# Kernel tuning notes

Hardware: AMD Instinct MI355X
Metric: run time of the kernel (lower is better)

Reference implementation:

```python
import jax, jax.numpy as jnp
import numpy as np

B, S, D_MODEL, H = 2, 2048, 2048, 16
DQK = D_MODEL // H            # 128
DV = D_MODEL * 2 // H // 3    # 85 (GLU branch)
SCALE = DQK ** -0.5
ROPE_BASE = 10000.0


def apply_rope(x):
    # x: [B, S, H, D], NeoX-style half rotation
    D = x.shape[-1]
    half = D // 2
    inv_freq = 1.0 / (ROPE_BASE ** (jnp.arange(half, dtype=jnp.float32) / half))
    ang = jnp.arange(x.shape[1], dtype=jnp.float32)[:, None] * inv_freq[None, :]  # [S, half]
    cos = jnp.cos(ang)[None, :, None, :]
    sin = jnp.sin(ang)[None, :, None, :]
    x1, x2 = x[..., :half], x[..., half:]
    return jnp.concatenate([x1 * cos - x2 * sin, x2 * cos + x1 * sin], axis=-1)


def setup_inputs() -> dict:
    key = jax.random.key(0)
    ks = jax.random.split(key, 12)
    init = lambda k, shape, fan_in: jax.random.uniform(k, shape, jnp.float32, -1.0, 1.0) * (fan_in ** -0.5)
    q = jax.random.normal(ks[0], (B, S, D_MODEL), jnp.float32)
    k = jax.random.normal(ks[1], (B, S, D_MODEL), jnp.float32)
    v = jax.random.normal(ks[2], (B, S, D_MODEL), jnp.float32)
    # causal boolean mask: True = masked (upper triangle)
    mask = jnp.triu(jnp.ones((S, S), dtype=bool), k=1)
    Wq = init(ks[3], (D_MODEL, DQK * H), D_MODEL)
    bq = init(ks[4], (DQK * H,), D_MODEL)
    Wk = init(ks[5], (D_MODEL, DQK * H), D_MODEL)
    bk = init(ks[6], (DQK * H,), D_MODEL)
    Wv = init(ks[7], (D_MODEL, DV * H * 2), D_MODEL)
    bv = init(ks[8], (DV * H * 2,), D_MODEL)
    Wo = init(ks[9], (DV * H, D_MODEL), DV * H)
    bo = init(ks[10], (D_MODEL,), DV * H)
    return {"q": q, "k": k, "v": v, "mask": mask,
            "Wq": Wq, "bq": bq, "Wk": Wk, "bk": bk,
            "Wv": Wv, "bv": bv, "Wo": Wo, "bo": bo}


def reference(q, k, v, mask, Wq, bq, Wk, bk, Wv, bv, Wo, bo):
    qp = q @ Wq + bq                      # [B,S,H*DQK]
    kp = k @ Wk + bk                      # [B,S,H*DQK]
    vp = v @ Wv + bv                      # [B,S,2*H*DV]
    # GLU over the FULL last dim (matches torch chunk(2, dim=-1) before unflatten)
    half = DV * H
    vg = vp[..., :half] * jax.nn.silu(vp[..., half:])   # [B,S,H*DV]
    qh = qp.reshape(B, S, H, DQK)
    kh = kp.reshape(B, S, H, DQK)
    vh = vg.reshape(B, S, H, DV)
    qh = apply_rope(qh)
    kh = apply_rope(kh)
    # [B,H,S,D]
    qh = qh.transpose(0, 2, 1, 3)
    kh = kh.transpose(0, 2, 1, 3)
    vh = vh.transpose(0, 2, 1, 3)
    score = jnp.einsum('bhqd,bhkd->bhqk', qh, kh) * SCALE  # [B,H,S,S]
    score = jnp.where(mask[None, None, :, :], -jnp.inf, score)
    attn = jax.nn.softmax(score, axis=-1)
    o = jnp.einsum('bhqk,bhkd->bhqd', attn, vh)            # [B,H,S,DV]
    o = o.transpose(0, 2, 1, 3).reshape(B, S, H * DV)
    return o @ Wo + bo                                     # [B,S,D_MODEL]
```

## Files before the change

kernel.cpp:

```cpp
#include <hip/hip_runtime.h>
#include <cstdint>
#include <cmath>

typedef __bf16 bf16;
typedef __bf16 bf16x8 __attribute__((ext_vector_type(8)));
typedef float f32x4 __attribute__((ext_vector_type(4)));

#define B_      2
#define S_      2048
#define H_      16
#define DQK_    128
#define DV_     85
#define DVP_    96
#define DMODEL_ 2048
#define NKV_    1360
#define KH_     1536
#define NV_     2720
#define NVP_    2816
#define SCALE_  0.08838834764831845f
#define QSCALE_ 0.12752044442215615f
#define M2_     16.0f

__device__ __forceinline__ void lds_cp16(const void* g, void* l) {
    __builtin_amdgcn_global_load_lds(
        (const __attribute__((address_space(1))) unsigned int*)(uintptr_t)g,
        (__attribute__((address_space(3))) unsigned int*)(uintptr_t)l,
        16, 0, 0);
}

__global__ __launch_bounds__(256) void detect_dtype(const unsigned int* __restrict__ w,
                                                    int* __restrict__ flag) {
    __shared__ int cnt;
    if (threadIdx.x == 0) cnt = 0;
    __syncthreads();
    unsigned v = w[threadIdx.x];
    unsigned e = (v >> 7) & 0xFFu;
    if (e > 100u && e < 140u) atomicAdd(&cnt, 1);
    __syncthreads();
    if (threadIdx.x == 0) *flag = (cnt >= 200) ? 1 : 0;
}

__global__ __launch_bounds__(256) void norm_mat(const void* __restrict__ src, bf16* __restrict__ dst,
                                                const int* __restrict__ flag, long n8) {
    long i = (long)blockIdx.x * 256 + threadIdx.x;
    if (i >= n8) return;
    if (*flag) {
        ((bf16x8*)dst)[i] = ((const bf16x8*)src)[i];
    } else {
        const float* s = (const float*)src;
        bf16x8 v;
#pragma unroll
        for (int j = 0; j < 8; ++j) v[j] = (bf16)s[i * 8 + j];
        ((bf16x8*)dst)[i] = v;
    }
}

__global__ __launch_bounds__(256) void norm_bias4(
    const void* __restrict__ s0, const void* __restrict__ s1,
    const void* __restrict__ s2, const void* __restrict__ s3,
    float* __restrict__ d0, float* __restrict__ d1,
    float* __restrict__ d2, float* __restrict__ d3,
    const int* __restrict__ flag) {
    int j = blockIdx.x * 256 + threadIdx.x;
    const void* s; float* d;
    if (j < DMODEL_) { s = s0; d = d0; }
    else if ((j -= DMODEL_) < DMODEL_) { s = s1; d = d1; }
    else if ((j -= DMODEL_) < NV_) { s = s2; d = d2; }
    else if ((j -= NV_) < DMODEL_) { s = s3; d = d3; }
    else return;
    d[j] = (*flag) ? (float)((const bf16*)s)[j] : ((const float*)s)[j];
}

__global__ __launch_bounds__(256) void transpose_pad_dyn(
    const void* __restrict__ in, bf16* __restrict__ out, const int* __restrict__ flag,
    int R, int C, int Rp, int Cp) {
    __shared__ bf16 tile[32][33];
    const bool isbf = (*flag != 0);
    int r0 = blockIdx.x * 32, c0 = blockIdx.y * 32;
    int tx = threadIdx.x, ty = threadIdx.y;
#pragma unroll
    for (int i = 0; i < 32; i += 8) {
        int r = r0 + ty + i, c = c0 + tx;
        bf16 v = (bf16)0.0f;
        if (r < R && c < C) {
            size_t idx = (size_t)r * C + c;
            v = isbf ? ((const bf16*)in)[idx] : (bf16)((const float*)in)[idx];
        }
        tile[ty + i][tx] = v;
    }
    __syncthreads();
#pragma unroll
    for (int i = 0; i < 32; i += 8) {
        int oc = c0 + ty + i, orr = r0 + tx;
        if (oc < Cp && orr < Rp) out[(size_t)oc * Rp + orr] = tile[tx][ty + i];
    }
}

__global__ __launch_bounds__(256) void transpose_wo_dyn(
    const void* __restrict__ in, bf16* __restrict__ out, const int* __restrict__ flag) {
    __shared__ bf16 tile[32][33];
    const bool isbf = (*flag != 0);
    int k0 = blockIdx.x * 32, n0 = blockIdx.y * 32;
    int tx = threadIdx.x, ty = threadIdx.y;
#pragma unroll
    for (int i = 0; i < 32; i += 8) {
        int k = k0 + ty + i, c = n0 + tx;
        int hh = k / DVP_, dd = k - hh * DVP_;
        bf16 v = (bf16)0.0f;
        if (dd < DV_) {
            size_t idx = (size_t)(hh * DV_ + dd) * DMODEL_ + c;
            v = isbf ? ((const bf16*)in)[idx] : (bf16)((const float*)in)[idx];
        }
        tile[ty + i][tx] = v;
    }
    __syncthreads();
#pragma unroll
    for (int i = 0; i < 32; i += 8) {
        int n = n0 + ty + i, k = k0 + tx;
        out[(size_t)n * KH_ + k] = tile[tx][ty + i];
    }
}

__global__ __launch_bounds__(256) void gemm_bt(
    const bf16* __restrict__ A, const bf16* __restrict__ Bt,
    const float* __restrict__ bias, bf16* __restrict__ C,
    int M, int N, int K, int Nreal, int ldc) {
    __shared__ bf16 As[128 * 32];
    __shared__ bf16 Bs[128 * 32];
    const int t = threadIdx.x, lane = t & 63, w = t >> 6;
    const int m0 = blockIdx.x * 128, n0 = blockIdx.y * 128;
    const int wm = (w >> 1) * 64, wn = (w & 1) * 64;
    const int fm = lane & 15, quad = lane >> 4, fk = quad * 8;
    const int srow = lane >> 2, scol = (lane & 3) * 8;
    f32x4 acc[4][4] = {};
    for (int k0 = 0; k0 < K; k0 += 32) {
        __syncthreads();
#pragma unroll
        for (int j = 0; j < 2; ++j) {
            int c = j * 4 + w;
            lds_cp16(A + (size_t)(m0 + c * 16 + srow) * K + k0 + scol, &As[c * 512]);
            lds_cp16(Bt + (size_t)(n0 + c * 16 + srow) * K + k0 + scol, &Bs[c * 512]);
        }
        __syncthreads();
        bf16x8 af[4], bfr[4];
#pragma unroll
        for (int i = 0; i < 4; ++i) {
            af[i]  = *(const bf16x8*)&As[(wm + i * 16 + fm) * 32 + fk];
            bfr[i] = *(const bf16x8*)&Bs[(wn + i * 16 + fm) * 32 + fk];
        }
#pragma unroll
        for (int i = 0; i < 4; ++i)
#pragma unroll
            for (int jn = 0; jn < 4; ++jn)
                acc[i][jn] = __builtin_amdgcn_mfma_f32_16x16x32_bf16(af[i], bfr[jn], acc[i][jn], 0, 0, 0);
    }
#pragma unroll
    for (int jn = 0; jn < 4; ++jn) {
        int col = n0 + wn + jn * 16 + fm;
        if (col >= Nreal) continue;
        float bv = bias[col];
#pragma unroll
        for (int i = 0; i < 4; ++i) {
            int rowb = m0 + wm + i * 16 + quad * 4;
#pragma unroll
            for (int r = 0; r < 4; ++r)
                C[(size_t)(rowb + r) * ldc + col] = (bf16)(acc[i][jn][r] + bv);
        }
    }
}

__global__ __launch_bounds__(256) void gemm_bt_oh(
    const bf16* __restrict__ Oh, const bf16* __restrict__ Bt,
    const float* __restrict__ bias, bf16* __restrict__ C, float* __restrict__ Cf,
    const int* __restrict__ outflag) {
    __shared__ bf16 As[128 * 32];
    __shared__ bf16 Bs[128 * 32];
    const int t = threadIdx.x, lane = t & 63, w = t >> 6;
    const int m0 = blockIdx.x * 128, n0 = blockIdx.y * 128;
    const int wm = (w >> 1) * 64, wn = (w & 1) * 64;
    const int fm = lane & 15, quad = lane >> 4, fk = quad * 8;
    const int srow = lane >> 2, scol = (lane & 3) * 8;
    f32x4 acc[4][4] = {};
    for (int k0 = 0; k0 < KH_; k0 += 32) {
        __syncthreads();
#pragma unroll
        for (int j = 0; j < 2; ++j) {
            int c = j * 4 + w;
            int m = m0 + c * 16 + srow;
            int k = k0 + scol;
            int hh = k / DVP_, dd = k - hh * DVP_;
            const bf16* ga = Oh + ((size_t)((m >> 11) * H_ + hh) * S_ + (m & (S_ - 1))) * DVP_ + dd;
            lds_cp16(ga, &As[c * 512]);
            lds_cp16(Bt + (size_t)(n0 + c * 16 + srow) * KH_ + k0 + scol, &Bs[c * 512]);
        }
        __syncthreads();
        bf16x8 af[4], bfr[4];
#pragma unroll
        for (int i = 0; i < 4; ++i) {
            af[i]  = *(const bf16x8*)&As[(wm + i * 16 + fm) * 32 + fk];
            bfr[i] = *(const bf16x8*)&Bs[(wn + i * 16 + fm) * 32 + fk];
        }
#pragma unroll
        for (int i = 0; i < 4; ++i)
#pragma unroll
            for (int jn = 0; jn < 4; ++jn)
                acc[i][jn] = __builtin_amdgcn_mfma_f32_16x16x32_bf16(af[i], bfr[jn], acc[i][jn], 0, 0, 0);
    }
    bool bf16out = (*outflag != 0);
#pragma unroll
    for (int jn = 0; jn < 4; ++jn) {
        int col = n0 + wn + jn * 16 + fm;
        float bv = bias[col];
#pragma unroll
        for (int i = 0; i < 4; ++i) {
            int rowb = m0 + wm + i * 16 + quad * 4;
            if (bf16out) {
#pragma unroll
                for (int r = 0; r < 4; ++r)
                    C[(size_t)(rowb + r) * DMODEL_ + col] = (bf16)(acc[i][jn][r] + bv);
            } else {
#pragma unroll
                for (int r = 0; r < 4; ++r)
                    Cf[(size_t)(rowb + r) * DMODEL_ + col] = acc[i][jn][r] + bv;
            }
        }
    }
}

__global__ __launch_bounds__(256) void rope_tr(const bf16* __restrict__ src, bf16* __restrict__ dst,
                                               float scale) {
    int idx = blockIdx.x * 256 + threadIdx.x;
    int d = idx & 63;
    int h = (idx >> 6) & 15;
    int s = (idx >> 10) & (S_ - 1);
    int b = idx >> 21;
    const bf16* p = src + ((size_t)(b * S_ + s) * DMODEL_ + h * DQK_);
    float x1 = (float)p[d], x2 = (float)p[d + 64];
    float ang = (float)s * exp2f(-(float)d * (13.287712379549449f / 64.0f));
    float sn, cs;
    sincosf(ang, &sn, &cs);
    bf16* q = dst + ((size_t)(b * H_ + h) * S_ + s) * DQK_;
    q[d]      = (bf16)((x1 * cs - x2 * sn) * scale);
    q[d + 64] = (bf16)((x2 * cs + x1 * sn) * scale);
}

__global__ __launch_bounds__(256) void swiglu_tr2(const bf16* __restrict__ vp, bf16* __restrict__ vt) {
    __shared__ bf16 tile[32][33];
    const int bh = blockIdx.x, b = bh >> 4, h = bh & 15;
    const int s0 = blockIdx.y * 32, d0 = blockIdx.z * 32;
    const int tx = threadIdx.x, ty = threadIdx.y;
#pragma unroll
    for (int i = 0; i < 32; i += 8) {
        int s = s0 + ty + i, d = d0 + tx;
        float val = 0.0f;
        if (d < DV_) {
            size_t row = (size_t)(b * S_ + s) * NV_ + h * DV_ + d;
            float a = (float)vp[row];
            float g = (float)vp[row + NKV_];
            val = a * g / (1.0f + __expf(-g));
        } else if (d == 95) {
            val = 1.0f;
        }
        tile[ty + i][tx] = (bf16)val;
    }
    __syncthreads();
#pragma unroll
    for (int i = 0; i < 32; i += 8) {
        int d = d0 + ty + i, s = s0 + tx;
        vt[((size_t)bh * DVP_ + d) * S_ + s] = tile[tx][ty + i];
    }
}

__global__ __launch_bounds__(256) void attn_split(
    const bf16* __restrict__ qt, const bf16* __restrict__ kt,
    const bf16* __restrict__ vt,
    bf16* __restrict__ Opart, float* __restrict__ lpart) {
    const int bh = blockIdx.x, qb = blockIdx.y, split = blockIdx.z;
    if (split * 8 > qb) return;
    __shared__ bf16 Ks[64 * 128];
    __shared__ bf16 Vs[96 * 64];
    __shared__ bf16 plds[4][16 * 72];
    const int t = threadIdx.x, lane = t & 63, w = t >> 6;
    const int fm = lane & 15, quad = lane >> 4;
    const int h = bh & 15, b = bh >> 4;
    const int q0 = qb * 64 + w * 16;
    const int g = qb >> 3;
    const int pidx = bh * 80 + 4 * g * (g + 1) + (qb & 7) * (g + 1) + split;

    const bf16* qbase = qt + ((size_t)(b * H_ + h) * S_ + q0 + fm) * DQK_ + quad * 8;
    bf16x8 aq[4];
#pragma unroll
    for (int kb = 0; kb < 4; ++kb) aq[kb] = *(const bf16x8*)(qbase + kb * 32);
    const bf16* kbase = kt + (size_t)(b * H_ + h) * S_ * DQK_;
    const bf16* vbase = vt + (size_t)(b * H_ + h) * DVP_ * S_;

    const float NEG_INF = -__builtin_inff();
    f32x4 oacc[6] = {};
    bf16* pl = &plds[w][0];

    const int t0 = split * 8;
    const int t1 = min(t0 + 8, qb + 1);
    for (int it = t0; it < t1; ++it) {
        const int k0 = it * 64;
        __syncthreads();
#pragma unroll
        for (int iw = 0; iw < 4; ++iw) {
            int flat = (w * 4 + iw) * 64 + lane;
            int r = flat >> 4, c = (flat & 15) ^ (r & 15);
            lds_cp16(kbase + (size_t)(k0 + r) * DQK_ + c * 8, &Ks[(w * 4 + iw) * 512]);
        }
#pragma unroll
        for (int iw = 0; iw < 3; ++iw) {
            int flat = (w * 3 + iw) * 64 + lane;
            int r = flat >> 3, c = (flat & 7) ^ (r & 7);
            lds_cp16(vbase + (size_t)r * S_ + k0 + c * 8, &Vs[(w * 3 + iw) * 512]);
        }
        __syncthreads();
        f32x4 sc[4] = {};
#pragma unroll
        for (int nt = 0; nt < 4; ++nt) {
            if (k0 + nt * 16 <= q0 + 15) {
                const int row16 = (nt * 16 + fm) * 16;
#pragma unroll
                for (int kb = 0; kb < 4; ++kb) {
                    const bf16* kp = &Ks[(row16 + ((kb * 4 + quad) ^ fm)) * 8];
                    sc[nt] = __builtin_amdgcn_mfma_f32_16x16x32_bf16(aq[kb], *(const bf16x8*)kp, sc[nt], 0, 0, 0);
                }
            }
        }
        if (it == qb) {
#pragma unroll
            for (int nt = 0; nt < 4; ++nt) {
                int col = k0 + nt * 16 + fm;
#pragma unroll
                for (int r = 0; r < 4; ++r) {
                    int rowq = q0 + quad * 4 + r;
                    if (col > rowq) sc[nt][r] = NEG_INF;
                }
            }
        }
#pragma unroll
        for (int nt = 0; nt < 4; ++nt)
#pragma unroll
            for (int r = 0; r < 4; ++r)
                pl[(quad * 4 + r) * 72 + nt * 16 + fm] =
                    (bf16)__builtin_amdgcn_exp2f(sc[nt][r] - M2_);
        asm volatile("s_waitcnt lgkmcnt(0)" ::: "memory");
        bf16x8 pa0 = *(const bf16x8*)(pl + fm * 72 + quad * 8);
        bf16x8 pa1 = *(const bf16x8*)(pl + fm * 72 + 32 + quad * 8);
#pragma unroll
        for (int n2 = 0; n2 < 6; ++n2) {
            int row8 = (n2 * 16 + fm) * 8;
            const bf16* v0 = &Vs[(row8 + (quad ^ (fm & 7))) * 8];
            const bf16* v1 = &Vs[(row8 + ((4 + quad) ^ (fm & 7))) * 8];
            oacc[n2] = __builtin_amdgcn_mfma_f32_16x16x32_bf16(pa0, *(const bf16x8*)v0, oacc[n2], 0, 0, 0);
            oacc[n2] = __builtin_amdgcn_mfma_f32_16x16x32_bf16(pa1, *(const bf16x8*)v1, oacc[n2], 0, 0, 0);
        }
    }
    float lv[4], inv_l[4];
#pragma unroll
    for (int r = 0; r < 4; ++r) {
        lv[r] = __shfl(oacc[5][r], (lane & 48) | 15, 64);
        inv_l[r] = (lv[r] > 0.f) ? 1.0f / lv[r] : 0.0f;
    }
    if (fm == 0) {
#pragma unroll
        for (int r = 0; r < 4; ++r) {
            int row = w * 16 + quad * 4 + r;
            lpart[(size_t)pidx * 64 + row] = lv[r];
        }
    }
#pragma unroll
    for (int n2 = 0; n2 < 6; ++n2)
#pragma unroll
        for (int r = 0; r < 4; ++r) {
            int row = w * 16 + quad * 4 + r;
            Opart[((size_t)pidx * 64 + row) * DVP_ + n2 * 16 + fm] = (bf16)(oacc[n2][r] * inv_l[r]);
        }
}

__global__ __launch_bounds__(256) void attn_combine2(
    const bf16* __restrict__ Opart, const float* __restrict__ lpart,
    bf16* __restrict__ oh) {
    const int bh = blockIdx.x, qb = blockIdx.y;
    const int g = qb >> 3, nact = g + 1;
    const int pidx0 = bh * 80 + 4 * g * (g + 1) + (qb & 7) * (g + 1);
    const int t = threadIdx.x;
#pragma unroll
    for (int i = 0; i < 3; ++i) {
        int idx = i * 256 + t;
        int row = idx / 12, ch = idx - row * 12;
        float W = 0.f, wgt[4];
        for (int p = 0; p < nact; ++p) {
            wgt[p] = lpart[(size_t)(pidx0 + p) * 64 + row];
            W += wgt[p];
        }
        float invW = (W > 0.f) ? 1.0f / W : 0.0f;
        float acc[8] = {};
        for (int p = 0; p < nact; ++p) {
            bf16x8 v = *(const bf16x8*)&Opart[((size_t)(pidx0 + p) * 64 + row) * DVP_ + ch * 8];
#pragma unroll
            for (int j = 0; j < 8; ++j) acc[j] += wgt[p] * (float)v[j];
        }
        bf16x8 o8;
#pragma unroll
        for (int j = 0; j < 8; ++j) o8[j] = (bf16)(acc[j] * invW);
        *(bf16x8*)&oh[((size_t)bh * S_ + qb * 64 + row) * DVP_ + ch * 8] = o8;
    }
}

extern "C" void kernel_launch(void* const* d_in, const int* in_sizes, int n_in,
                              void* d_out, int out_size, void* d_ws, size_t ws_size,
                              hipStream_t stream) {
    const void* qin = d_in[0];
    const void* kin = d_in[1];
    const void* vin = d_in[2];
    const void* Wq = d_in[4];
    const void* bq = d_in[5];
    const void* Wk = d_in[6];
    const void* bk = d_in[7];
    const void* Wv = d_in[8];
    const void* bv = d_in[9];
    const void* Wo = d_in[10];
    const void* bo = d_in[11];

    char* ws = (char*)d_ws;
    size_t off = 0;
    auto alloc = [&](size_t bytes) {
        char* p = ws + off;
        off += ((bytes + 255) & ~(size_t)255);
        return (void*)p;
    };
    bf16* qt   = (bf16*)alloc((size_t)B_ * H_ * S_ * DQK_ * 2);
    bf16* ktp  = (bf16*)alloc((size_t)B_ * H_ * S_ * DQK_ * 2);
    bf16* vtp  = (bf16*)alloc((size_t)B_ * H_ * DVP_ * S_ * 2);
    bf16* oh   = (bf16*)alloc((size_t)B_ * H_ * S_ * DVP_ * 2);
    bf16* wT   = (bf16*)alloc((size_t)NVP_ * DMODEL_ * 2);
    bf16* proj = (bf16*)alloc((size_t)B_ * S_ * NV_ * 2);
    bf16* scr  = (bf16*)alloc((size_t)B_ * S_ * DMODEL_ * 2);
    float* bqf = (float*)alloc(DMODEL_ * 4);
    float* bkf = (float*)alloc(DMODEL_ * 4);
    float* bvf = (float*)alloc(NV_ * 4);
    float* bof = (float*)alloc(DMODEL_ * 4);
    int*  flag = (int*)alloc(256);
    bf16*  Opart = proj;
    float* lpart = (float*)((char*)proj + (size_t)2560 * 64 * DVP_ * 2);

    dim3 tb(32, 8);
    auto nblk = [](long n8) { return (int)((n8 + 255) / 256); };
    long n8_x = (long)B_ * S_ * DMODEL_ / 8;

    detect_dtype<<<1, 256, 0, stream>>>((const unsigned int*)qin, flag);
    norm_bias4<<<(3 * DMODEL_ + NV_ + 255) / 256, 256, 0, stream>>>(
        bq, bk, bv, bo, bqf, bkf, bvf, bof, flag);

    transpose_pad_dyn<<<dim3(DMODEL_ / 32, DMODEL_ / 32), tb, 0, stream>>>(Wq, wT, flag, DMODEL_, DMODEL_, DMODEL_, DMODEL_);
    norm_mat<<<nblk(n8_x), 256, 0, stream>>>(qin, scr, flag, n8_x);
    gemm_bt<<<dim3(32, 16), 256, 0, stream>>>(scr, wT, bqf, proj, 4096, 2048, 2048, 2048, 2048);
    rope_tr<<<(B_ * S_ * H_ * 64) / 256, 256, 0, stream>>>(proj, qt, QSCALE_);

    transpose_pad_dyn<<<dim3(DMODEL_ / 32, DMODEL_ / 32), tb, 0, stream>>>(Wk, wT, flag, DMODEL_, DMODEL_, DMODEL_, DMODEL_);
    norm_mat<<<nblk(n8_x), 256, 0, stream>>>(kin, scr, flag, n8_x);
    gemm_bt<<<dim3(32, 16), 256, 0, stream>>>(scr, wT, bkf, proj, 4096, 2048, 2048, 2048, 2048);
    rope_tr<<<(B_ * S_ * H_ * 64) / 256, 256, 0, stream>>>(proj, ktp, 1.0f);

    transpose_pad_dyn<<<dim3(DMODEL_ / 32, NVP_ / 32), tb, 0, stream>>>(Wv, wT, flag, DMODEL_, NV_, DMODEL_, NVP_);
    norm_mat<<<nblk(n8_x), 256, 0, stream>>>(vin, scr, flag, n8_x);
    gemm_bt<<<dim3(32, NVP_ / 128), 256, 0, stream>>>(scr, wT, bvf, proj, 4096, NVP_, 2048, NV_, NV_);
    swiglu_tr2<<<dim3(B_ * H_, S_ / 32, 3), tb, 0, stream>>>(proj, vtp);

    transpose_wo_dyn<<<dim3(KH_ / 32, DMODEL_ / 32), tb, 0, stream>>>(Wo, wT, flag);

    attn_split<<<dim3(32, 32, 4), 256, 0, stream>>>(qt, ktp, vtp, Opart, lpart);
    attn_combine2<<<dim3(32, 32), 256, 0, stream>>>(Opart, lpart, oh);

    gemm_bt_oh<<<dim3(32, 16), 256, 0, stream>>>(oh, wT, bof, (bf16*)d_out, (float*)d_out, flag);
}
```

Baseline: 559.9 us.

## Fuse Q/K projection GEMMs with RoPE epilogue into one batched launch

Adds a gemm_qk_rope kernel that computes the Q and K projections in a single launch, using blockIdx.z to select Q or K. RoPE, the bias and the Q scale are applied in an LDS-staged epilogue that writes directly to the head-major transposed layout. This removes the two separate rope_tr passes and their projected intermediates' global round trip, and doubles the grid so more blocks run at once. It also restructures the workspace into fixed aliased regions so Q and K inputs and weights can coexist. The cost is extra LDS for the epilogue, which may limit occupancy, and the use of the fast __sincosf intrinsic in place of sincosf.

```diff
diff --git a/kernel.cpp b/kernel.cpp
--- a/kernel.cpp
+++ b/kernel.cpp
@@ -20,6 +20,7 @@
 #define SCALE_  0.08838834764831845f
 #define QSCALE_ 0.12752044442215615f
 #define M2_     16.0f
+#define L2_10K_ 13.287712379549449f
 
 __device__ __forceinline__ void lds_cp16(const void* g, void* l) {
     __builtin_amdgcn_global_load_lds(
@@ -121,6 +122,90 @@
     }
 }
 
+__global__ __launch_bounds__(256) void gemm_qk_rope(
+    const bf16* __restrict__ Aq, const bf16* __restrict__ Ak,
+    const bf16* __restrict__ Btq, const bf16* __restrict__ Btk,
+    const float* __restrict__ bq, const float* __restrict__ bk,
+    bf16* __restrict__ qt, bf16* __restrict__ ktp) {
+    __shared__ bf16 As[128 * 32];
+    __shared__ bf16 Bs[128 * 32];
+    __shared__ bf16 ep[64 * 132];
+    const int z = blockIdx.z;
+    const bf16* A    = z ? Ak  : Aq;
+    const bf16* Bt   = z ? Btk : Btq;
+    const float* bias = z ? bk : bq;
+    bf16* dst        = z ? ktp : qt;
+    const float qs   = z ? 1.0f : QSCALE_;
+    const int t = threadIdx.x, lane = t & 63, w = t >> 6;
+    const int m0 = blockIdx.x * 128, n0 = blockIdx.y * 128;
+    const int wm = (w >> 1) * 64, wn = (w & 1) * 64;
+    const int fm = lane & 15, quad = lane >> 4, fk = quad * 8;
+    const int srow = lane >> 2, scol = (lane & 3) * 8;
+    f32x4 acc[4][4] = {};
+    for (int k0 = 0; k0 < DMODEL_; k0 += 32) {
+        __syncthreads();
+#pragma unroll
+        for (int j = 0; j < 2; ++j) {
+            int c = j * 4 + w;
+            lds_cp16(A + (size_t)(m0 + c * 16 + srow) * DMODEL_ + k0 + scol, &As[c * 512]);
+            lds_cp16(Bt + (size_t)(n0 + c * 16 + srow) * DMODEL_ + k0 + scol, &Bs[c * 512]);
+        }
+        __syncthreads();
+        bf16x8 af[4], bfr[4];
+#pragma unroll
+        for (int i = 0; i < 4; ++i) {
+            af[i]  = *(const bf16x8*)&As[(wm + i * 16 + fm) * 32 + fk];
+            bfr[i] = *(const bf16x8*)&Bs[(wn + i * 16 + fm) * 32 + fk];
+        }
+#pragma unroll
+        for (int i = 0; i < 4; ++i)
+#pragma unroll
+            for (int jn = 0; jn < 4; ++jn)
+                acc[i][jn] = __builtin_amdgcn_mfma_f32_16x16x32_bf16(af[i], bfr[jn], acc[i][jn], 0, 0, 0);
+    }
+    const int h = blockIdx.y;
+    const int b = m0 >> 11, s_base = m0 & (S_ - 1);
+    float bv[4];
+#pragma unroll
+    for (int jn = 0; jn < 4; ++jn) bv[jn] = bias[n0 + wn + jn * 16 + fm];
+    bf16* dbase = dst + (size_t)(b * H_ + h) * S_ * DQK_;
+#pragma unroll
+    for (int ph = 0; ph < 2; ++ph) {
+        if ((w >> 1) == ph) {
+#pragma unroll
+            for (int i = 0; i < 4; ++i)
+#pragma unroll
+                for (int jn = 0; jn < 4; ++jn)
+#pragma unroll
+                    for (int r = 0; r < 4; ++r)
+                        ep[(i * 16 + quad * 4 + r) * 132 + wn + jn * 16 + fm] =
+                            (bf16)(acc[i][jn][r] + bv[jn]);
+        }
+        __syncthreads();
+#pragma unroll
+        for (int it2 = 0; it2 < 4; ++it2) {
+            int task = it2 * 256 + t;
+            int lr = task >> 4, ch = task & 15;
+            int s = s_base + ph * 64 + lr;
+            bf16x8 v = *(const bf16x8*)&ep[lr * 132 + ch * 8];
+            bf16x8 u = *(const bf16x8*)&ep[lr * 132 + ((ch * 8) ^ 64)];
+            bf16x8 o8;
+#pragma unroll
+            for (int j = 0; j < 8; ++j) {
+                int d = ch * 8 + j, dd = d & 63;
+                float ang = (float)s * exp2f(-(float)dd * (L2_10K_ / 64.0f));
+                float sn, cs;
+                __sincosf(ang, &sn, &cs);
+                float x = (float)v[j], y = (float)u[j];
+                float ov = (d < 64) ? (x * cs - y * sn) : (x * cs + y * sn);
+                o8[j] = (bf16)(ov * qs);
+            }
+            *(bf16x8*)&dbase[(size_t)s * DQK_ + ch * 8] = o8;
+        }
+        __syncthreads();
+    }
+}
+
 __global__ __launch_bounds__(256) void gemm_bt(
     const bf16* __restrict__ A, const bf16* __restrict__ Bt,
     const float* __restrict__ bias, bf16* __restrict__ C,
@@ -225,23 +310,6 @@
             }
         }
     }
-}
-
-__global__ __launch_bounds__(256) void rope_tr(const bf16* __restrict__ src, bf16* __restrict__ dst,
-                                               float scale) {
-    int idx = blockIdx.x * 256 + threadIdx.x;
-    int d = idx & 63;
-    int h = (idx >> 6) & 15;
-    int s = (idx >> 10) & (S_ - 1);
-    int b = idx >> 21;
-    const bf16* p = src + ((size_t)(b * S_ + s) * DMODEL_ + h * DQK_);
-    float x1 = (float)p[d], x2 = (float)p[d + 64];
-    float ang = (float)s * exp2f(-(float)d * (13.287712379549449f / 64.0f));
-    float sn, cs;
-    sincosf(ang, &sn, &cs);
-    bf16* q = dst + ((size_t)(b * H_ + h) * S_ + s) * DQK_;
-    q[d]      = (bf16)((x1 * cs - x2 * sn) * scale);
-    q[d + 64] = (bf16)((x2 * cs + x1 * sn) * scale);
 }
 
 __global__ __launch_bounds__(256) void swiglu_tr2(const bf16* __restrict__ vp, bf16* __restrict__ vt) {
@@ -425,26 +493,26 @@
     const void* bo = d_in[11];
 
     char* ws = (char*)d_ws;
-    size_t off = 0;
-    auto alloc = [&](size_t bytes) {
-        char* p = ws + off;
-        off += ((bytes + 255) & ~(size_t)255);
-        return (void*)p;
-    };
-    bf16* qt   = (bf16*)alloc((size_t)B_ * H_ * S_ * DQK_ * 2);
-    bf16* ktp  = (bf16*)alloc((size_t)B_ * H_ * S_ * DQK_ * 2);
-    bf16* vtp  = (bf16*)alloc((size_t)B_ * H_ * DVP_ * S_ * 2);
-    bf16* oh   = (bf16*)alloc((size_t)B_ * H_ * S_ * DVP_ * 2);
-    bf16* wT   = (bf16*)alloc((size_t)NVP_ * DMODEL_ * 2);
-    bf16* proj = (bf16*)alloc((size_t)B_ * S_ * NV_ * 2);
-    bf16* scr  = (bf16*)alloc((size_t)B_ * S_ * DMODEL_ * 2);
-    float* bqf = (float*)alloc(DMODEL_ * 4);
-    float* bkf = (float*)alloc(DMODEL_ * 4);
-    float* bvf = (float*)alloc(NV_ * 4);
-    float* bof = (float*)alloc(DMODEL_ * 4);
-    int*  flag = (int*)alloc(256);
-    bf16*  Opart = proj;
-    float* lpart = (float*)((char*)proj + (size_t)2560 * 64 * DVP_ * 2);
+    bf16* qt   = (bf16*)(ws);
+    bf16* ktp  = (bf16*)(ws + 16777216);
+    char* R1   = ws + 33554432;
+    bf16* scrq = (bf16*)(R1);
+    bf16* scrk = (bf16*)(R1 + 16777216);
+    bf16* wTq  = (bf16*)(R1 + 33554432);
+    bf16* wTk  = (bf16*)(R1 + 41943040);
+    bf16* scrv  = (bf16*)(R1);
+    bf16* wTv   = (bf16*)(R1 + 16777216);
+    bf16* projv = (bf16*)(R1 + 28311552);
+    bf16*  wTo   = (bf16*)(R1);
+    bf16*  Opart = (bf16*)(R1 + 6291456);
+    float* lpart = (float*)(R1 + 37748736);
+    bf16* vtp = (bf16*)(ws + 84148224);
+    bf16* oh  = (bf16*)(ws + 96731136);
+    float* bqf = (float*)(ws + 109314048);
+    float* bkf = bqf + DMODEL_;
+    float* bvf = bkf + DMODEL_;
+    float* bof = bvf + NV_;
+    int*  flag = (int*)(bof + DMODEL_);
 
     dim3 tb(32, 8);
     auto nblk = [](long n8) { return (int)((n8 + 255) / 256); };
@@ -454,25 +522,21 @@
     norm_bias4<<<(3 * DMODEL_ + NV_ + 255) / 256, 256, 0, stream>>>(
         bq, bk, bv, bo, bqf, bkf, bvf, bof, flag);
 
-    transpose_pad_dyn<<<dim3(DMODEL_ / 32, DMODEL_ / 32), tb, 0, stream>>>(Wq, wT, flag, DMODEL_, DMODEL_, DMODEL_, DMODEL_);
-    norm_mat<<<nblk(n8_x), 256, 0, stream>>>(qin, scr, flag, n8_x);
-    gemm_bt<<<dim3(32, 16), 256, 0, stream>>>(scr, wT, bqf, proj, 4096, 2048, 2048, 2048, 2048);
-    rope_tr<<<(B_ * S_ * H_ * 64) / 256, 256, 0, stream>>>(proj, qt, QSCALE_);
-
-    transpose_pad_dyn<<<dim3(DMODEL_ / 32, DMODEL_ / 32), tb, 0, stream>>>(Wk, wT, flag, DMODEL_, DMODEL_, DMODEL_, DMODEL_);
-    norm_mat<<<nblk(n8_x), 256, 0, stream>>>(kin, scr, flag, n8_x);
-    gemm_bt<<<dim3(32, 16), 256, 0, stream>>>(scr, wT, bkf, proj, 4096, 2048, 2048, 2048, 2048);
-    rope_tr<<<(B_ * S_ * H_ * 64) / 256, 256, 0, stream>>>(proj, ktp, 1.0f);
-
-    transpose_pad_dyn<<<dim3(DMODEL_ / 32, NVP_ / 32), tb, 0, stream>>>(Wv, wT, flag, DMODEL_, NV_, DMODEL_, NVP_);
-    norm_mat<<<nblk(n8_x), 256, 0, stream>>>(vin, scr, flag, n8_x);
-    gemm_bt<<<dim3(32, NVP_ / 128), 256, 0, stream>>>(scr, wT, bvf, proj, 4096, NVP_, 2048, NV_, NV_);
-    swiglu_tr2<<<dim3(B_ * H_, S_ / 32, 3), tb, 0, stream>>>(proj, vtp);
-
-    transpose_wo_dyn<<<dim3(KH_ / 32, DMODEL_ / 32), tb, 0, stream>>>(Wo, wT, flag);
+    norm_mat<<<nblk(n8_x), 256, 0, stream>>>(qin, scrq, flag, n8_x);
+    norm_mat<<<nblk(n8_x), 256, 0, stream>>>(kin, scrk, flag, n8_x);
+    transpose_pad_dyn<<<dim3(64, 64), tb, 0, stream>>>(Wq, wTq, flag, DMODEL_, DMODEL_, DMODEL_, DMODEL_);
+    transpose_pad_dyn<<<dim3(64, 64), tb, 0, stream>>>(Wk, wTk, flag, DMODEL_, DMODEL_, DMODEL_, DMODEL_);
+    gemm_qk_rope<<<dim3(32, 16, 2), 256, 0, stream>>>(scrq, scrk, wTq, wTk, bqf, bkf, qt, ktp);
+
+    norm_mat<<<nblk(n8_x), 256, 0, stream>>>(vin, scrv, flag, n8_x);
+    transpose_pad_dyn<<<dim3(64, NVP_ / 32), tb, 0, stream>>>(Wv, wTv, flag, DMODEL_, NV_, DMODEL_, NVP_);
+    gemm_bt<<<dim3(32, NVP_ / 128), 256, 0, stream>>>(scrv, wTv, bvf, projv, 4096, NVP_, 2048, NV_, NV_);
+    swiglu_tr2<<<dim3(B_ * H_, S_ / 32, 3), tb, 0, stream>>>(projv, vtp);
+
+    transpose_wo_dyn<<<dim3(KH_ / 32, DMODEL_ / 32), tb, 0, stream>>>(Wo, wTo, flag);
 
     attn_split<<<dim3(32, 32, 4), 256, 0, stream>>>(qt, ktp, vtp, Opart, lpart);
     attn_combine2<<<dim3(32, 32), 256, 0, stream>>>(Opart, lpart, oh);
 
-    gemm_bt_oh<<<dim3(32, 16), 256, 0, stream>>>(oh, wT, bof, (bf16*)d_out, (float*)d_out, flag);
-}
+    gemm_bt_oh<<<dim3(32, 16), 256, 0, stream>>>(oh, wTo, bof, (bf16*)d_out, (float*)d_out, flag);
+}
```

After: 528.9 us. 1.06x faster.
